# Optimization experiments

Hardware: AMD Instinct MI355X
Metric: run time of the kernel (lower is better)

The kernel has to match this reference:

```python
import jax, jax.numpy as jnp
import numpy as np

B, C, H, W = 4, 64, 128, 128

def conv1x1(x, w, b):
    # x: [B,Ci,H,W], w: [Co,Ci], b: [Co]
    return jnp.einsum('bchw,oc->bohw', x, w) + b[None, :, None, None]

def setup_inputs() -> dict:
    key = jax.random.key(0)
    ks = jax.random.split(key, 10)
    d = {}
    d['x'] = jax.random.normal(ks[0], (B, C, H, W), dtype=jnp.float32)
    # patchmerging params: LayerNorm(4C) + Linear(4C -> C)
    d['pm_gamma'] = jnp.ones((4 * C,), jnp.float32)
    d['pm_beta'] = jnp.zeros((4 * C,), jnp.float32)
    d['pm_w'] = jax.random.normal(ks[1], (C, 4 * C), jnp.float32) * 0.02
    d['pm_b'] = jnp.zeros((C,), jnp.float32)
    # 1x1 convs: conv2..conv6 are C->C, conv1 is 2C->C
    for i, n in enumerate(['2', '3', '4', '5', '6']):
        d['w' + n] = jax.random.normal(ks[2 + i], (C, C), jnp.float32) * 0.05
        d['b' + n] = jnp.zeros((C,), jnp.float32)
    d['w1'] = jax.random.normal(ks[7], (C, 2 * C), jnp.float32) * 0.05
    d['b1'] = jnp.zeros((C,), jnp.float32)
    return d

def reference(x, pm_gamma, pm_beta, pm_w, pm_b,
              w1, b1, w2, b2, w3, b3, w4, b4, w5, b5, w6, b6):
    Bx, Cx, Hx, Wx = x.shape
    Hh, Wh = Hx // 2, Wx // 2
    N = Hh * Wh
    # ---- patch merging ----
    x0 = x[:, :, 0::2, 0::2]
    x1_ = x[:, :, 1::2, 0::2]
    x2_ = x[:, :, 0::2, 1::2]
    x3_ = x[:, :, 1::2, 1::2]
    m = jnp.concatenate([x0, x1_, x2_, x3_], axis=1)        # [B,4C,Hh,Wh]
    t = m.reshape(Bx, 4 * Cx, N).transpose(0, 2, 1)          # [B,N,4C]
    mu = t.mean(-1, keepdims=True)
    var = t.var(-1, keepdims=True)
    t = (t - mu) / jnp.sqrt(var + 1e-5) * pm_gamma + pm_beta  # LayerNorm eps=1e-5
    t = t @ pm_w.T + pm_b                                     # [B,N,C]
    c1 = t.transpose(0, 2, 1).reshape(Bx, Cx, Hh, Wh)
    # ---- spatial attention (PAM-style) ----
    q = conv1x1(c1, w2, b2).reshape(Bx, Cx, N)
    k = conv1x1(c1, w3, b3).reshape(Bx, Cx, N)
    v = conv1x1(c1, w4, b4).reshape(Bx, Cx, N)
    qk1 = jax.nn.softmax(jnp.einsum('bcn,bcm->bnm', q, k), axis=-1)  # [B,N,N]
    # torch: out1 = v @ qk1.permute(0,2,1) -> out1[b,c,j] = sum_i v[b,c,i]*qk1[b,j,i]
    out1 = jnp.einsum('bci,bji->bcj', v, qk1).reshape(Bx, Cx, Hh, Wh)
    # ---- channel attention (CAM-style) ----
    q2 = conv1x1(c1, w5, b5).reshape(Bx, Cx, N)
    k2 = conv1x1(c1, w6, b6).reshape(Bx, Cx, N)
    qk2 = jax.nn.softmax(jnp.einsum('bcn,bdn->bcd', q2, k2), axis=-1)  # [B,C,C]
    out2 = jnp.einsum('bcd,bdn->bcn', qk2, v).reshape(Bx, Cx, Hh, Wh)
    # ---- fuse, 1x1 conv, bilinear upsample x2 (align_corners=False), residual ----
    out = jnp.concatenate([out1, out2], axis=1)              # [B,2C,Hh,Wh]
    out = conv1x1(out, w1, b1)                               # [B,C,Hh,Wh]
    out = jax.image.resize(out, (Bx, Cx, Hx, Wx), method='bilinear')
    return out + x
```

## Files before the change

### kernel.cpp

```cpp
#include <hip/hip_runtime.h>

typedef __attribute__((ext_vector_type(8))) short bf16x8;
typedef __attribute__((ext_vector_type(4))) float fx4;

struct __attribute__((aligned(8))) sh4 { short x, y, z, w; };

#define OPART_B   0u
#define ML_B      8388608u
#define SMALL_B   8650752u
#define L2M_B     12845056u
#define C1B_B     12910592u
#define QB_B      15007744u
#define KB_B      17104896u
#define VCN_B     19202048u
#define VNC_B     21299200u
#define Q2B_B     23396352u
#define K2B_B     25493504u
#define CATB_B    27590656u
#define P2B_B     31784960u
#define PMB_B     31817728u
#define W2B_B     31850496u
#define W3B_B     31858688u
#define W4B_B     31866880u
#define W5B_B     31875072u
#define W6B_B     31883264u
#define W1B_B     31891456u

static __device__ __forceinline__ short f2bf(float f) {
  unsigned u = __float_as_uint(f);
  unsigned r = (u + 0x7FFFu + ((u >> 16) & 1u)) >> 16;
  return (short)r;
}
static __device__ __forceinline__ float bf2f(short s) {
  return __uint_as_float(((unsigned)(unsigned short)s) << 16);
}

__global__ __launch_bounds__(256) void prep_kernel(
    const float* __restrict__ pm_w, const float* __restrict__ w2,
    const float* __restrict__ w3,  const float* __restrict__ w4,
    const float* __restrict__ w5,  const float* __restrict__ w6,
    const float* __restrict__ w1,  char* __restrict__ wsb)
{
  int tid = blockIdx.x * 256 + threadIdx.x;
  ((short*)(wsb + PMB_B))[tid] = f2bf(pm_w[tid]);
  if (tid < 4096) {
    ((short*)(wsb + W2B_B))[tid] = f2bf(w2[tid]);
    ((short*)(wsb + W3B_B))[tid] = f2bf(w3[tid]);
    ((short*)(wsb + W4B_B))[tid] = f2bf(w4[tid]);
    ((short*)(wsb + W5B_B))[tid] = f2bf(w5[tid]);
    ((short*)(wsb + W6B_B))[tid] = f2bf(w6[tid]);
  }
  if (tid < 8192) ((short*)(wsb + W1B_B))[tid] = f2bf(w1[tid]);
  ((float*)(wsb + L2M_B))[tid] = 0.0f;
}

__global__ __launch_bounds__(256) void patchln_kernel(
    const float* __restrict__ x, const float* __restrict__ gamma,
    const float* __restrict__ beta, const short* __restrict__ pmb,
    const float* __restrict__ pm_b, short* __restrict__ c1b)
{
  __shared__ short tnb[32*264];
  __shared__ float red_s[512];
  __shared__ float mu_s[32], rs_s[32];
  const int b   = blockIdx.y;
  const int i   = blockIdx.x >> 1;
  const int jh  = blockIdx.x & 1;
  const int tid = threadIdx.x;
  const int j   = tid & 31;
  const int g8  = tid >> 5;
  const int jj  = jh*32 + j;

  float vals[32];
  float sm = 0.f, sq = 0.f;
  #pragma unroll
  for (int k = 0; k < 16; ++k) {
    int p  = g8*16 + k;
    int cc = p & 63, di = p >> 6;
    float2 v2 = *(const float2*)&x[((size_t)(b*64 + cc)*128 + 2*i + di)*128 + 2*jj];
    vals[2*k]   = v2.x;
    vals[2*k+1] = v2.y;
    sm += v2.x + v2.y; sq += v2.x*v2.x + v2.y*v2.y;
  }
  red_s[g8*32 + j] = sm;
  red_s[256 + g8*32 + j] = sq;
  __syncthreads();
  if (tid < 32) {
    float s0 = 0.f, q0 = 0.f;
    #pragma unroll
    for (int g = 0; g < 8; ++g) { s0 += red_s[g*32 + tid]; q0 += red_s[256 + g*32 + tid]; }
    float mu  = s0 * (1.0f/256.0f);
    float var = q0 * (1.0f/256.0f) - mu*mu;
    mu_s[tid] = mu;
    rs_s[tid] = rsqrtf(var + 1e-5f);
  }
  __syncthreads();
  {
    float mu = mu_s[j], rs = rs_s[j];
    #pragma unroll
    for (int k = 0; k < 16; ++k) {
      int p  = g8*16 + k;
      int ca = p, cb = p + 128;
      tnb[j*264 + ca] = f2bf((vals[2*k]   - mu)*rs*gamma[ca] + beta[ca]);
      tnb[j*264 + cb] = f2bf((vals[2*k+1] - mu)*rs*gamma[cb] + beta[cb]);
    }
  }
  __syncthreads();

  const int w    = tid >> 6;
  const int lane = tid & 63;
  const int L15  = lane & 15;
  const int quad = lane >> 4;
  fx4 d0 = {0.f,0.f,0.f,0.f}, d1 = {0.f,0.f,0.f,0.f};
  #pragma unroll
  for (int kc = 0; kc < 8; ++kc) {
    bf16x8 a  = *(const bf16x8*)&pmb[(w*16 + L15)*256 + kc*32 + quad*8];
    bf16x8 bf0 = *(const bf16x8*)&tnb[(L15)*264      + kc*32 + quad*8];
    bf16x8 bf1 = *(const bf16x8*)&tnb[(16 + L15)*264 + kc*32 + quad*8];
    d0 = __builtin_amdgcn_mfma_f32_16x16x32_bf16(a, bf0, d0, 0, 0, 0);
    d1 = __builtin_amdgcn_mfma_f32_16x16x32_bf16(a, bf1, d1, 0, 0, 0);
  }
  const int obase = w*16 + quad*4;
  float bias0 = pm_b[obase], bias1 = pm_b[obase+1], bias2 = pm_b[obase+2], bias3 = pm_b[obase+3];
  const int gn0 = i*64 + jh*32 + L15;
  sh4 s0; s0.x = f2bf(d0[0]+bias0); s0.y = f2bf(d0[1]+bias1); s0.z = f2bf(d0[2]+bias2); s0.w = f2bf(d0[3]+bias3);
  sh4 s1; s1.x = f2bf(d1[0]+bias0); s1.y = f2bf(d1[1]+bias1); s1.z = f2bf(d1[2]+bias2); s1.w = f2bf(d1[3]+bias3);
  *(sh4*)&c1b[((size_t)b*4096 + gn0)*64 + obase]      = s0;
  *(sh4*)&c1b[((size_t)b*4096 + gn0 + 16)*64 + obase] = s1;
}

__global__ __launch_bounds__(256) void proj5_kernel(
    const short* __restrict__ c1b,
    const short* __restrict__ w2b, const short* __restrict__ w3b, const short* __restrict__ w4b,
    const short* __restrict__ w5b, const short* __restrict__ w6b,
    const float* __restrict__ b2, const float* __restrict__ b3, const float* __restrict__ b4,
    const float* __restrict__ b5, const float* __restrict__ b6,
    short* __restrict__ qb, short* __restrict__ kb,
    short* __restrict__ vcn, short* __restrict__ vnc,
    short* __restrict__ q2b, short* __restrict__ k2b)
{
  const int b    = blockIdx.y;
  const int tid  = threadIdx.x;
  const int w    = tid >> 6;
  const int nsub = w & 1;
  const int pg   = w >> 1;
  const int lane = tid & 63;
  const int L15  = lane & 15;
  const int quad = lane >> 4;
  const int gn   = blockIdx.x*32 + nsub*16 + L15;

  bf16x8 bf0 = *(const bf16x8*)&c1b[((size_t)b*4096 + gn)*64 + quad*8];
  bf16x8 bf1 = *(const bf16x8*)&c1b[((size_t)b*4096 + gn)*64 + quad*8 + 32];

  if (pg == 0) {
    const short* wp[3] = {w2b, w3b, w4b};
    const float* bp[3] = {b2, b3, b4};
    #pragma unroll
    for (int p = 0; p < 3; ++p) {
      #pragma unroll
      for (int mt = 0; mt < 4; ++mt) {
        bf16x8 a0 = *(const bf16x8*)&wp[p][(mt*16 + L15)*64 + quad*8];
        bf16x8 a1 = *(const bf16x8*)&wp[p][(mt*16 + L15)*64 + quad*8 + 32];
        fx4 d = {0.f,0.f,0.f,0.f};
        d = __builtin_amdgcn_mfma_f32_16x16x32_bf16(a0, bf0, d, 0, 0, 0);
        d = __builtin_amdgcn_mfma_f32_16x16x32_bf16(a1, bf1, d, 0, 0, 0);
        const int obase = mt*16 + quad*4;
        float r0 = d[0] + bp[p][obase];
        float r1 = d[1] + bp[p][obase+1];
        float r2 = d[2] + bp[p][obase+2];
        float r3 = d[3] + bp[p][obase+3];
        sh4 s; s.x = f2bf(r0); s.y = f2bf(r1); s.z = f2bf(r2); s.w = f2bf(r3);
        short* dst = (p == 0) ? qb : (p == 1) ? kb : vnc;
        *(sh4*)&dst[((size_t)b*4096 + gn)*64 + obase] = s;
        if (p == 2) {
          vcn[((size_t)b*64 + obase + 0)*4096 + gn] = s.x;
          vcn[((size_t)b*64 + obase + 1)*4096 + gn] = s.y;
          vcn[((size_t)b*64 + obase + 2)*4096 + gn] = s.z;
          vcn[((size_t)b*64 + obase + 3)*4096 + gn] = s.w;
        }
      }
    }
  } else {
    const short* wp[2] = {w5b, w6b};
    const float* bp[2] = {b5, b6};
    #pragma unroll
    for (int p = 0; p < 2; ++p) {
      short* dst = (p == 0) ? q2b : k2b;
      #pragma unroll
      for (int mt = 0; mt < 4; ++mt) {
        bf16x8 a0 = *(const bf16x8*)&wp[p][(mt*16 + L15)*64 + quad*8];
        bf16x8 a1 = *(const bf16x8*)&wp[p][(mt*16 + L15)*64 + quad*8 + 32];
        fx4 d = {0.f,0.f,0.f,0.f};
        d = __builtin_amdgcn_mfma_f32_16x16x32_bf16(a0, bf0, d, 0, 0, 0);
        d = __builtin_amdgcn_mfma_f32_16x16x32_bf16(a1, bf1, d, 0, 0, 0);
        const int obase = mt*16 + quad*4;
        dst[((size_t)b*64 + obase + 0)*4096 + gn] = f2bf(d[0] + bp[p][obase]);
        dst[((size_t)b*64 + obase + 1)*4096 + gn] = f2bf(d[1] + bp[p][obase+1]);
        dst[((size_t)b*64 + obase + 2)*4096 + gn] = f2bf(d[2] + bp[p][obase+2]);
        dst[((size_t)b*64 + obase + 3)*4096 + gn] = f2bf(d[3] + bp[p][obase+3]);
      }
    }
  }
}

__global__ __launch_bounds__(256) void flash_mfma_kernel(
    const short* __restrict__ Qb, const short* __restrict__ Kb,
    const short* __restrict__ Vb, short* __restrict__ opart, float* __restrict__ lsum)
{
  __shared__ short lds_s[20480];
  short* ktb = lds_s;
  short* vsb = lds_s + 8192;
  short* ps  = lds_s + 16384;

  const int b    = blockIdx.z;
  const int s    = blockIdx.y;
  const int q0   = blockIdx.x << 6;
  const int t0   = s << 4;
  const int tid  = threadIdx.x;
  const int w    = tid >> 6;
  const int lane = tid & 63;
  const int L15  = lane & 15;
  const int quad = lane >> 4;

  const short* Qg = Qb + (size_t)b*4096*64;
  const short* Kg = Kb + (size_t)b*4096*64;
  const short* Vg = Vb + (size_t)b*4096*64;

  bf16x8 qa0 = *(const bf16x8*)(Qg + (size_t)(q0 + w*16 + L15)*64 + quad*8);
  bf16x8 qa1 = *(const bf16x8*)(Qg + (size_t)(q0 + w*16 + L15)*64 + quad*8 + 32);

  bf16x8 ones;
  #pragma unroll
  for (int u = 0; u < 8; ++u) ones[u] = (short)0x3F80;

  const int si  = tid >> 2;
  const int scb = (tid & 3) * 2;
  const int s0k = scb ^ (si & 7);
  const int s1k = s0k ^ 1;

  {
    const int i0 = t0 << 6;
    bf16x8 kr0 = *(const bf16x8*)(Kg + (size_t)(i0 + si)*64 + scb*8);
    bf16x8 kr1 = *(const bf16x8*)(Kg + (size_t)(i0 + si)*64 + scb*8 + 8);
    bf16x8 vr0 = *(const bf16x8*)(Vg + (size_t)si*4096 + i0 + (tid&3)*16);
    bf16x8 vr1 = *(const bf16x8*)(Vg + (size_t)si*4096 + i0 + (tid&3)*16 + 8);
    *(bf16x8*)(ktb + si*64 + s0k*8) = kr0;
    *(bf16x8*)(ktb + si*64 + s1k*8) = kr1;
    *(bf16x8*)(vsb + si*64 + s0k*8) = vr0;
    *(bf16x8*)(vsb + si*64 + s1k*8) = vr1;
  }
  __syncthreads();

  fx4 oacc[4] = {{0.f,0.f,0.f,0.f},{0.f,0.f,0.f,0.f},{0.f,0.f,0.f,0.f},{0.f,0.f,0.f,0.f}};
  fx4 lacc   = {0.f,0.f,0.f,0.f};

  const int cbx0 = quad       ^ (L15 & 7);
  const int cbx1 = (quad + 4) ^ (L15 & 7);
  const int jq   = (quad*4) & 7;

  for (int t = 0; t < 16; ++t) {
    const short* kt = ktb + (t & 1)*4096;
    const short* vv = vsb + (t & 1)*4096;
    short* ktn = ktb + ((t + 1) & 1)*4096;
    short* vsn = vsb + ((t + 1) & 1)*4096;

    bf16x8 kr0, kr1, vr0, vr1;
    const bool pf = (t < 15);
    if (pf) {
      const int i0n = (t0 + t + 1) << 6;
      kr0 = *(const bf16x8*)(Kg + (size_t)(i0n + si)*64 + scb*8);
      kr1 = *(const bf16x8*)(Kg + (size_t)(i0n + si)*64 + scb*8 + 8);
      vr0 = *(const bf16x8*)(Vg + (size_t)si*4096 + i0n + (tid&3)*16);
      vr1 = *(const bf16x8*)(Vg + (size_t)si*4096 + i0n + (tid&3)*16 + 8);
    }

    fx4 sreg[4] = {{0.f,0.f,0.f,0.f},{0.f,0.f,0.f,0.f},{0.f,0.f,0.f,0.f},{0.f,0.f,0.f,0.f}};
    #pragma unroll
    for (int nt = 0; nt < 4; ++nt) {
      bf16x8 bk = *(const bf16x8*)(kt + (nt*16 + L15)*64 + cbx0*8);
      sreg[nt] = __builtin_amdgcn_mfma_f32_16x16x32_bf16(qa0, bk, sreg[nt], 0, 0, 0);
    }
    #pragma unroll
    for (int nt = 0; nt < 4; ++nt) {
      bf16x8 bk = *(const bf16x8*)(kt + (nt*16 + L15)*64 + cbx1*8);
      sreg[nt] = __builtin_amdgcn_mfma_f32_16x16x32_bf16(qa1, bk, sreg[nt], 0, 0, 0);
    }

    #pragma unroll
    for (int r = 0; r < 4; ++r) {
      const int j   = w*16 + quad*4 + r;
      const int js  = (jq + r) & 7;
      #pragma unroll
      for (int nt = 0; nt < 4; ++nt) {
        float e = __expf(sreg[nt][r]);
        const int slot = (nt*2 + (L15 >> 3)) ^ js;
        ps[j*64 + slot*8 + (L15 & 7)] = f2bf(e);
      }
    }

    bf16x8 pa0 = *(const bf16x8*)(ps + (w*16 + L15)*64 + (( quad      ^ (L15 & 7))*8));
    bf16x8 pa1 = *(const bf16x8*)(ps + (w*16 + L15)*64 + (((quad + 4) ^ (L15 & 7))*8));

    lacc = __builtin_amdgcn_mfma_f32_16x16x32_bf16(pa0, ones, lacc, 0, 0, 0);
    lacc = __builtin_amdgcn_mfma_f32_16x16x32_bf16(pa1, ones, lacc, 0, 0, 0);

    #pragma unroll
    for (int ct = 0; ct < 4; ++ct) {
      bf16x8 vb0 = *(const bf16x8*)(vv + (ct*16 + L15)*64 + cbx0*8);
      oacc[ct] = __builtin_amdgcn_mfma_f32_16x16x32_bf16(pa0, vb0, oacc[ct], 0, 0, 0);
      bf16x8 vb1 = *(const bf16x8*)(vv + (ct*16 + L15)*64 + cbx1*8);
      oacc[ct] = __builtin_amdgcn_mfma_f32_16x16x32_bf16(pa1, vb1, oacc[ct], 0, 0, 0);
    }

    if (pf) {
      *(bf16x8*)(ktn + si*64 + s0k*8) = kr0;
      *(bf16x8*)(ktn + si*64 + s1k*8) = kr1;
      *(bf16x8*)(vsn + si*64 + s0k*8) = vr0;
      *(bf16x8*)(vsn + si*64 + s1k*8) = vr1;
    }
    __syncthreads();
  }

  const size_t rowbase = ((size_t)(b*4 + s)*4096 + q0);
  #pragma unroll
  for (int ct = 0; ct < 4; ++ct) {
    #pragma unroll
    for (int r = 0; r < 4; ++r) {
      opart[(rowbase + w*16 + quad*4 + r)*64 + ct*16 + L15] = f2bf(oacc[ct][r]);
    }
  }
  if (L15 == 0) {
    #pragma unroll
    for (int r = 0; r < 4; ++r) {
      lsum[rowbase + w*16 + quad*4 + r] = lacc[r];
    }
  }
}

__global__ __launch_bounds__(256) void merge_kernel(
    const short* __restrict__ opart, const float* __restrict__ lsum, short* __restrict__ catb)
{
  int g  = blockIdx.x*256 + threadIdx.x;
  int b  = g >> 14;
  int r  = g & 16383;
  int n  = r >> 2;
  int c0 = (r & 3) * 16;
  float l0 = lsum[((size_t)(b*4 + 0)*4096) + n];
  float l1 = lsum[((size_t)(b*4 + 1)*4096) + n];
  float l2 = lsum[((size_t)(b*4 + 2)*4096) + n];
  float l3 = lsum[((size_t)(b*4 + 3)*4096) + n];
  float invL = 1.0f / (l0 + l1 + l2 + l3);
  bf16x8 oa, ob;
  float va[8] = {0,0,0,0,0,0,0,0}, vb[8] = {0,0,0,0,0,0,0,0};
  #pragma unroll
  for (int sp = 0; sp < 4; ++sp) {
    bf16x8 pa = *(const bf16x8*)&opart[(((size_t)(b*4+sp)*4096) + n)*64 + c0];
    bf16x8 pb = *(const bf16x8*)&opart[(((size_t)(b*4+sp)*4096) + n)*64 + c0 + 8];
    #pragma unroll
    for (int u = 0; u < 8; ++u) { va[u] += bf2f(pa[u]); vb[u] += bf2f(pb[u]); }
  }
  #pragma unroll
  for (int u = 0; u < 8; ++u) { oa[u] = f2bf(va[u]*invL); ob[u] = f2bf(vb[u]*invL); }
  *(bf16x8*)&catb[((size_t)b*4096 + n)*128 + c0]     = oa;
  *(bf16x8*)&catb[((size_t)b*4096 + n)*128 + c0 + 8] = ob;
}

__global__ __launch_bounds__(256) void corr_kernel(
    const short* __restrict__ q2b, const short* __restrict__ k2b, float* __restrict__ L2M)
{
  const int b    = blockIdx.y;
  const int n0   = blockIdx.x * 128;
  const int tid  = threadIdx.x;
  const int w    = tid >> 6;
  const int lane = tid & 63;
  const int L15  = lane & 15;
  const int quad = lane >> 4;
  const short* qg = q2b + (size_t)b*64*4096;
  const short* kg = k2b + (size_t)b*64*4096;
  fx4 D[4] = {{0.f,0.f,0.f,0.f},{0.f,0.f,0.f,0.f},{0.f,0.f,0.f,0.f},{0.f,0.f,0.f,0.f}};
  #pragma unroll
  for (int kc = 0; kc < 4; ++kc) {
    bf16x8 a = *(const bf16x8*)&qg[(w*16 + L15)*4096 + n0 + kc*32 + quad*8];
    #pragma unroll
    for (int nt = 0; nt < 4; ++nt) {
      bf16x8 bb = *(const bf16x8*)&kg[(nt*16 + L15)*4096 + n0 + kc*32 + quad*8];
      D[nt] = __builtin_amdgcn_mfma_f32_16x16x32_bf16(a, bb, D[nt], 0, 0, 0);
    }
  }
  float* Lb = L2M + (size_t)b*4096;
  #pragma unroll
  for (int nt = 0; nt < 4; ++nt)
    #pragma unroll
    for (int r = 0; r < 4; ++r)
      atomicAdd(&Lb[(w*16 + quad*4 + r)*64 + nt*16 + L15], D[nt][r]);
}

__global__ __launch_bounds__(64) void softmax64_kernel(
    const float* __restrict__ L, short* __restrict__ p2b)
{
  const int b = blockIdx.y, c = blockIdx.x, d = threadIdx.x;
  float v = L[(size_t)b*4096 + c*64 + d];
  float mx = v;
  mx = fmaxf(mx, __shfl_xor(mx, 1));
  mx = fmaxf(mx, __shfl_xor(mx, 2));
  mx = fmaxf(mx, __shfl_xor(mx, 4));
  mx = fmaxf(mx, __shfl_xor(mx, 8));
  mx = fmaxf(mx, __shfl_xor(mx, 16));
  mx = fmaxf(mx, __shfl_xor(mx, 32));
  float e = __expf(v - mx);
  float sm = e;
  sm += __shfl_xor(sm, 1);
  sm += __shfl_xor(sm, 2);
  sm += __shfl_xor(sm, 4);
  sm += __shfl_xor(sm, 8);
  sm += __shfl_xor(sm, 16);
  sm += __shfl_xor(sm, 32);
  p2b[(size_t)b*4096 + c*64 + d] = f2bf(e / sm);
}

__global__ __launch_bounds__(256) void out2_kernel(
    const short* __restrict__ p2b, const short* __restrict__ vnc, short* __restrict__ catb)
{
  const int b    = blockIdx.y;
  const int tid  = threadIdx.x;
  const int w    = tid >> 6;
  const int nsub = w & 1;
  const int mh   = w >> 1;
  const int lane = tid & 63;
  const int L15  = lane & 15;
  const int quad = lane >> 4;
  const int gn   = blockIdx.x*32 + nsub*16 + L15;

  bf16x8 bf0 = *(const bf16x8*)&vnc[((size_t)b*4096 + gn)*64 + quad*8];
  bf16x8 bf1 = *(const bf16x8*)&vnc[((size_t)b*4096 + gn)*64 + quad*8 + 32];
  #pragma unroll
  for (int mi = 0; mi < 2; ++mi) {
    const int mt = mh*2 + mi;
    bf16x8 a0 = *(const bf16x8*)&p2b[(size_t)b*4096 + (mt*16 + L15)*64 + quad*8];
    bf16x8 a1 = *(const bf16x8*)&p2b[(size_t)b*4096 + (mt*16 + L15)*64 + quad*8 + 32];
    fx4 d = {0.f,0.f,0.f,0.f};
    d = __builtin_amdgcn_mfma_f32_16x16x32_bf16(a0, bf0, d, 0, 0, 0);
    d = __builtin_amdgcn_mfma_f32_16x16x32_bf16(a1, bf1, d, 0, 0, 0);
    sh4 sv; sv.x = f2bf(d[0]); sv.y = f2bf(d[1]); sv.z = f2bf(d[2]); sv.w = f2bf(d[3]);
    *(sh4*)&catb[((size_t)b*4096 + gn)*128 + 64 + mt*16 + quad*4] = sv;
  }
}

__global__ __launch_bounds__(256) void conv_kernel(
    const short* __restrict__ catb, const short* __restrict__ w1b,
    const float* __restrict__ b1, float* __restrict__ sml)
{
  const int b    = blockIdx.y;
  const int tid  = threadIdx.x;
  const int w    = tid >> 6;
  const int nsub = w & 1;
  const int mh   = w >> 1;
  const int lane = tid & 63;
  const int L15  = lane & 15;
  const int quad = lane >> 4;
  const int gn   = blockIdx.x*32 + nsub*16 + L15;

  bf16x8 bfr[4];
  #pragma unroll
  for (int kc = 0; kc < 4; ++kc)
    bfr[kc] = *(const bf16x8*)&catb[((size_t)b*4096 + gn)*128 + kc*32 + quad*8];
  #pragma unroll
  for (int mi = 0; mi < 2; ++mi) {
    const int mt = mh*2 + mi;
    fx4 d = {0.f,0.f,0.f,0.f};
    #pragma unroll
    for (int kc = 0; kc < 4; ++kc) {
      bf16x8 a = *(const bf16x8*)&w1b[(mt*16 + L15)*128 + kc*32 + quad*8];
      d = __builtin_amdgcn_mfma_f32_16x16x32_bf16(a, bfr[kc], d, 0, 0, 0);
    }
    const int obase = mt*16 + quad*4;
    #pragma unroll
    for (int r = 0; r < 4; ++r)
      sml[((size_t)b*64 + obase + r)*4096 + gn] = d[r] + b1[obase + r];
  }
}

__global__ __launch_bounds__(256) void upsample_kernel(
    const float* __restrict__ sml, const float* __restrict__ x, float* __restrict__ out)
{
  int idx = blockIdx.x*256 + threadIdx.x;
  int J  = idx & 127;
  int I  = (idx >> 7) & 127;
  int bo = idx >> 14;
  int ih = I >> 1, jh = J >> 1;
  int i0, i1, j0, j1; float wi0, wi1, wj0, wj1;
  if (I & 1) { i0 = ih;                 i1 = (ih < 63) ? ih+1 : 63; wi0 = 0.75f; wi1 = 0.25f; }
  else       { i0 = (ih > 0) ? ih-1 : 0; i1 = ih;                   wi0 = 0.25f; wi1 = 0.75f; }
  if (J & 1) { j0 = jh;                 j1 = (jh < 63) ? jh+1 : 63; wj0 = 0.75f; wj1 = 0.25f; }
  else       { j0 = (jh > 0) ? jh-1 : 0; j1 = jh;                   wj0 = 0.25f; wj1 = 0.75f; }
  const float* sp = sml + (size_t)bo*4096;
  float r0 = wj0*sp[i0*64 + j0] + wj1*sp[i0*64 + j1];
  float r1 = wj0*sp[i1*64 + j0] + wj1*sp[i1*64 + j1];
  out[idx] = wi0*r0 + wi1*r1 + x[idx];
}

extern "C" void kernel_launch(void* const* d_in, const int* in_sizes, int n_in,
                              void* d_out, int out_size, void* d_ws, size_t ws_size,
                              hipStream_t stream) {
  const float* x     = (const float*)d_in[0];
  const float* gamma = (const float*)d_in[1];
  const float* beta  = (const float*)d_in[2];
  const float* pm_w  = (const float*)d_in[3];
  const float* pm_b  = (const float*)d_in[4];
  const float* w2 = (const float*)d_in[5];  const float* b2 = (const float*)d_in[6];
  const float* w3 = (const float*)d_in[7];  const float* b3 = (const float*)d_in[8];
  const float* w4 = (const float*)d_in[9];  const float* b4 = (const float*)d_in[10];
  const float* w5 = (const float*)d_in[11]; const float* b5 = (const float*)d_in[12];
  const float* w6 = (const float*)d_in[13]; const float* b6 = (const float*)d_in[14];
  const float* w1 = (const float*)d_in[15]; const float* b1 = (const float*)d_in[16];
  char* wsb  = (char*)d_ws;
  float* out = (float*)d_out;

  short* opart = (short*)(wsb + OPART_B);
  float* lsum  = (float*)(wsb + ML_B);
  float* sml   = (float*)(wsb + SMALL_B);
  float* l2m   = (float*)(wsb + L2M_B);
  short* c1b   = (short*)(wsb + C1B_B);
  short* qb    = (short*)(wsb + QB_B);
  short* kb    = (short*)(wsb + KB_B);
  short* vcn   = (short*)(wsb + VCN_B);
  short* vnc   = (short*)(wsb + VNC_B);
  short* q2b   = (short*)(wsb + Q2B_B);
  short* k2b   = (short*)(wsb + K2B_B);
  short* catb  = (short*)(wsb + CATB_B);
  short* p2b   = (short*)(wsb + P2B_B);
  short* pmb   = (short*)(wsb + PMB_B);
  short* w2b   = (short*)(wsb + W2B_B);
  short* w3b   = (short*)(wsb + W3B_B);
  short* w4b   = (short*)(wsb + W4B_B);
  short* w5b   = (short*)(wsb + W5B_B);
  short* w6b   = (short*)(wsb + W6B_B);
  short* w1b   = (short*)(wsb + W1B_B);

  prep_kernel<<<dim3(64), dim3(256), 0, stream>>>(pm_w, w2, w3, w4, w5, w6, w1, wsb);
  patchln_kernel<<<dim3(128,4), dim3(256), 0, stream>>>(x, gamma, beta, pmb, pm_b, c1b);
  proj5_kernel<<<dim3(128,4), dim3(256), 0, stream>>>(c1b, w2b, w3b, w4b, w5b, w6b,
      b2, b3, b4, b5, b6, qb, kb, vcn, vnc, q2b, k2b);
  flash_mfma_kernel<<<dim3(64,4,4), dim3(256), 0, stream>>>(qb, kb, vcn, opart, lsum);
  merge_kernel<<<dim3(256), dim3(256), 0, stream>>>(opart, lsum, catb);
  corr_kernel<<<dim3(32,4), dim3(256), 0, stream>>>(q2b, k2b, l2m);
  softmax64_kernel<<<dim3(64,4), dim3(64), 0, stream>>>(l2m, p2b);
  out2_kernel<<<dim3(128,4), dim3(256), 0, stream>>>(p2b, vnc, catb);
  conv_kernel<<<dim3(128,4), dim3(256), 0, stream>>>(catb, w1b, b1, sml);
  upsample_kernel<<<dim3(16384), dim3(256), 0, stream>>>(sml, x, out);
}
```

Measured before the change: 174.0 us.

## Restructure flash attention tiling and fuse merge, out2 and conv into tail kernel

The flash kernel now gives each block 128 query rows, each warp 32, and splits the KV range 8 ways instead of 4. K and V are read straight from global memory, with no LDS staging, double buffering or per-tile barriers, and the P/V operand roles are swapped so opart is written with vectorized stores. The merge, out2 and conv1x1 kernels are fused into a single tail kernel that builds the concat tile in LDS and writes the small output as bf16 in NC layout. The upsample then reads that bf16 buffer with strided gathers. This cuts launches and intermediate global traffic, at the cost of more partial-sum traffic, uncached global K/V reads, an extra bf16 rounding of the conv output, and a less accurate float-to-bf16 conversion for the exp values.

```diff
diff --git a/kernel.cpp b/kernel.cpp
--- a/kernel.cpp
+++ b/kernel.cpp
@@ -6,30 +6,32 @@
 struct __attribute__((aligned(8))) sh4 { short x, y, z, w; };
 
 #define OPART_B   0u
-#define ML_B      8388608u
-#define SMALL_B   8650752u
-#define L2M_B     12845056u
-#define C1B_B     12910592u
-#define QB_B      15007744u
-#define KB_B      17104896u
-#define VCN_B     19202048u
-#define VNC_B     21299200u
-#define Q2B_B     23396352u
-#define K2B_B     25493504u
-#define CATB_B    27590656u
-#define P2B_B     31784960u
-#define PMB_B     31817728u
-#define W2B_B     31850496u
-#define W3B_B     31858688u
-#define W4B_B     31866880u
-#define W5B_B     31875072u
-#define W6B_B     31883264u
-#define W1B_B     31891456u
+#define LSUM_B    16777216u
+#define SMALL_B   17301504u
+#define L2M_B     19398656u
+#define C1B_B     19464192u
+#define QB_B      21561344u
+#define KB_B      23658496u
+#define VCN_B     25755648u
+#define VNC_B     27852800u
+#define Q2B_B     29949952u
+#define K2B_B     32047104u
+#define P2B_B     34144256u
+#define PMB_B     34177024u
+#define W2B_B     34209792u
+#define W3B_B     34217984u
+#define W4B_B     34226176u
+#define W5B_B     34234368u
+#define W6B_B     34242560u
+#define W1B_B     34250752u
 
 static __device__ __forceinline__ short f2bf(float f) {
   unsigned u = __float_as_uint(f);
   unsigned r = (u + 0x7FFFu + ((u >> 16) & 1u)) >> 16;
   return (short)r;
+}
+static __device__ __forceinline__ short f2bf_fast(float f) {
+  return (short)((__float_as_uint(f) + 0x8000u) >> 16);
 }
 static __device__ __forceinline__ float bf2f(short s) {
   return __uint_as_float(((unsigned)(unsigned short)s) << 16);
@@ -202,166 +204,116 @@
   }
 }
 
-__global__ __launch_bounds__(256) void flash_mfma_kernel(
+__global__ __launch_bounds__(256) void flash_kernel(
     const short* __restrict__ Qb, const short* __restrict__ Kb,
-    const short* __restrict__ Vb, short* __restrict__ opart, float* __restrict__ lsum)
-{
-  __shared__ short lds_s[20480];
-  short* ktb = lds_s;
-  short* vsb = lds_s + 8192;
-  short* ps  = lds_s + 16384;
-
+    const short* __restrict__ Vcn, short* __restrict__ opart, float* __restrict__ lsum)
+{
+  __shared__ short ps[8192];
   const int b    = blockIdx.z;
   const int s    = blockIdx.y;
-  const int q0   = blockIdx.x << 6;
-  const int t0   = s << 4;
+  const int q0   = blockIdx.x << 7;
   const int tid  = threadIdx.x;
   const int w    = tid >> 6;
   const int lane = tid & 63;
   const int L15  = lane & 15;
   const int quad = lane >> 4;
-
-  const short* Qg = Qb + (size_t)b*4096*64;
-  const short* Kg = Kb + (size_t)b*4096*64;
-  const short* Vg = Vb + (size_t)b*4096*64;
-
-  bf16x8 qa0 = *(const bf16x8*)(Qg + (size_t)(q0 + w*16 + L15)*64 + quad*8);
-  bf16x8 qa1 = *(const bf16x8*)(Qg + (size_t)(q0 + w*16 + L15)*64 + quad*8 + 32);
+  const int jbase = w*32;
+
+  const short* Qg = Qb  + (size_t)b*262144;
+  const short* Kg = Kb  + (size_t)b*262144;
+  const short* Vg = Vcn + (size_t)b*262144;
+
+  bf16x8 qa[2][2];
+  #pragma unroll
+  for (int jt = 0; jt < 2; ++jt)
+    #pragma unroll
+    for (int h = 0; h < 2; ++h)
+      qa[jt][h] = *(const bf16x8*)(Qg + (size_t)(q0 + jbase + jt*16 + L15)*64 + h*32 + quad*8);
 
   bf16x8 ones;
   #pragma unroll
   for (int u = 0; u < 8; ++u) ones[u] = (short)0x3F80;
 
-  const int si  = tid >> 2;
-  const int scb = (tid & 3) * 2;
-  const int s0k = scb ^ (si & 7);
-  const int s1k = s0k ^ 1;
-
-  {
-    const int i0 = t0 << 6;
-    bf16x8 kr0 = *(const bf16x8*)(Kg + (size_t)(i0 + si)*64 + scb*8);
-    bf16x8 kr1 = *(const bf16x8*)(Kg + (size_t)(i0 + si)*64 + scb*8 + 8);
-    bf16x8 vr0 = *(const bf16x8*)(Vg + (size_t)si*4096 + i0 + (tid&3)*16);
-    bf16x8 vr1 = *(const bf16x8*)(Vg + (size_t)si*4096 + i0 + (tid&3)*16 + 8);
-    *(bf16x8*)(ktb + si*64 + s0k*8) = kr0;
-    *(bf16x8*)(ktb + si*64 + s1k*8) = kr1;
-    *(bf16x8*)(vsb + si*64 + s0k*8) = vr0;
-    *(bf16x8*)(vsb + si*64 + s1k*8) = vr1;
-  }
-  __syncthreads();
-
-  fx4 oacc[4] = {{0.f,0.f,0.f,0.f},{0.f,0.f,0.f,0.f},{0.f,0.f,0.f,0.f},{0.f,0.f,0.f,0.f}};
-  fx4 lacc   = {0.f,0.f,0.f,0.f};
-
-  const int cbx0 = quad       ^ (L15 & 7);
-  const int cbx1 = (quad + 4) ^ (L15 & 7);
-  const int jq   = (quad*4) & 7;
-
-  for (int t = 0; t < 16; ++t) {
-    const short* kt = ktb + (t & 1)*4096;
-    const short* vv = vsb + (t & 1)*4096;
-    short* ktn = ktb + ((t + 1) & 1)*4096;
-    short* vsn = vsb + ((t + 1) & 1)*4096;
-
-    bf16x8 kr0, kr1, vr0, vr1;
-    const bool pf = (t < 15);
-    if (pf) {
-      const int i0n = (t0 + t + 1) << 6;
-      kr0 = *(const bf16x8*)(Kg + (size_t)(i0n + si)*64 + scb*8);
-      kr1 = *(const bf16x8*)(Kg + (size_t)(i0n + si)*64 + scb*8 + 8);
-      vr0 = *(const bf16x8*)(Vg + (size_t)si*4096 + i0n + (tid&3)*16);
-      vr1 = *(const bf16x8*)(Vg + (size_t)si*4096 + i0n + (tid&3)*16 + 8);
-    }
-
-    fx4 sreg[4] = {{0.f,0.f,0.f,0.f},{0.f,0.f,0.f,0.f},{0.f,0.f,0.f,0.f},{0.f,0.f,0.f,0.f}};
+  fx4 oacc[2][4];
+  #pragma unroll
+  for (int jt = 0; jt < 2; ++jt)
+    #pragma unroll
+    for (int ct = 0; ct < 4; ++ct) oacc[jt][ct] = (fx4){0.f,0.f,0.f,0.f};
+  fx4 lacc[2] = {{0.f,0.f,0.f,0.f},{0.f,0.f,0.f,0.f}};
+
+  for (int t = 0; t < 8; ++t) {
+    const int i0 = (s*8 + t) << 6;
+
+    fx4 sreg[2][4];
+    #pragma unroll
+    for (int jt = 0; jt < 2; ++jt)
+      #pragma unroll
+      for (int nt = 0; nt < 4; ++nt) sreg[jt][nt] = (fx4){0.f,0.f,0.f,0.f};
     #pragma unroll
     for (int nt = 0; nt < 4; ++nt) {
-      bf16x8 bk = *(const bf16x8*)(kt + (nt*16 + L15)*64 + cbx0*8);
-      sreg[nt] = __builtin_amdgcn_mfma_f32_16x16x32_bf16(qa0, bk, sreg[nt], 0, 0, 0);
-    }
-    #pragma unroll
-    for (int nt = 0; nt < 4; ++nt) {
-      bf16x8 bk = *(const bf16x8*)(kt + (nt*16 + L15)*64 + cbx1*8);
-      sreg[nt] = __builtin_amdgcn_mfma_f32_16x16x32_bf16(qa1, bk, sreg[nt], 0, 0, 0);
-    }
-
-    #pragma unroll
-    for (int r = 0; r < 4; ++r) {
-      const int j   = w*16 + quad*4 + r;
-      const int js  = (jq + r) & 7;
-      #pragma unroll
-      for (int nt = 0; nt < 4; ++nt) {
-        float e = __expf(sreg[nt][r]);
-        const int slot = (nt*2 + (L15 >> 3)) ^ js;
-        ps[j*64 + slot*8 + (L15 & 7)] = f2bf(e);
+      const short* kp = Kg + (size_t)(i0 + nt*16 + L15)*64 + quad*8;
+      bf16x8 bk0 = *(const bf16x8*)kp;
+      bf16x8 bk1 = *(const bf16x8*)(kp + 32);
+      sreg[0][nt] = __builtin_amdgcn_mfma_f32_16x16x32_bf16(qa[0][0], bk0, sreg[0][nt], 0, 0, 0);
+      sreg[1][nt] = __builtin_amdgcn_mfma_f32_16x16x32_bf16(qa[1][0], bk0, sreg[1][nt], 0, 0, 0);
+      sreg[0][nt] = __builtin_amdgcn_mfma_f32_16x16x32_bf16(qa[0][1], bk1, sreg[0][nt], 0, 0, 0);
+      sreg[1][nt] = __builtin_amdgcn_mfma_f32_16x16x32_bf16(qa[1][1], bk1, sreg[1][nt], 0, 0, 0);
+    }
+
+    #pragma unroll
+    for (int jt = 0; jt < 2; ++jt)
+      #pragma unroll
+      for (int r = 0; r < 4; ++r) {
+        const int j  = jbase + jt*16 + quad*4 + r;
+        const int jk = j & 7;
+        #pragma unroll
+        for (int nt = 0; nt < 4; ++nt) {
+          float e = __expf(sreg[jt][nt][r]);
+          ps[j*64 + (((nt*2 + (L15 >> 3)) ^ jk) << 3) + (L15 & 7)] = f2bf_fast(e);
+        }
       }
-    }
-
-    bf16x8 pa0 = *(const bf16x8*)(ps + (w*16 + L15)*64 + (( quad      ^ (L15 & 7))*8));
-    bf16x8 pa1 = *(const bf16x8*)(ps + (w*16 + L15)*64 + (((quad + 4) ^ (L15 & 7))*8));
-
-    lacc = __builtin_amdgcn_mfma_f32_16x16x32_bf16(pa0, ones, lacc, 0, 0, 0);
-    lacc = __builtin_amdgcn_mfma_f32_16x16x32_bf16(pa1, ones, lacc, 0, 0, 0);
+
+    bf16x8 pb[2][2];
+    #pragma unroll
+    for (int jt = 0; jt < 2; ++jt) {
+      const int jrow = jbase + jt*16 + L15;
+      const int jk   = L15 & 7;
+      pb[jt][0] = *(const bf16x8*)&ps[jrow*64 + (((quad    ) ^ jk) << 3)];
+      pb[jt][1] = *(const bf16x8*)&ps[jrow*64 + (((quad + 4) ^ jk) << 3)];
+    }
+
+    #pragma unroll
+    for (int jt = 0; jt < 2; ++jt) {
+      lacc[jt] = __builtin_amdgcn_mfma_f32_16x16x32_bf16(ones, pb[jt][0], lacc[jt], 0, 0, 0);
+      lacc[jt] = __builtin_amdgcn_mfma_f32_16x16x32_bf16(ones, pb[jt][1], lacc[jt], 0, 0, 0);
+    }
 
     #pragma unroll
     for (int ct = 0; ct < 4; ++ct) {
-      bf16x8 vb0 = *(const bf16x8*)(vv + (ct*16 + L15)*64 + cbx0*8);
-      oacc[ct] = __builtin_amdgcn_mfma_f32_16x16x32_bf16(pa0, vb0, oacc[ct], 0, 0, 0);
-      bf16x8 vb1 = *(const bf16x8*)(vv + (ct*16 + L15)*64 + cbx1*8);
-      oacc[ct] = __builtin_amdgcn_mfma_f32_16x16x32_bf16(pa1, vb1, oacc[ct], 0, 0, 0);
-    }
-
-    if (pf) {
-      *(bf16x8*)(ktn + si*64 + s0k*8) = kr0;
-      *(bf16x8*)(ktn + si*64 + s1k*8) = kr1;
-      *(bf16x8*)(vsn + si*64 + s0k*8) = vr0;
-      *(bf16x8*)(vsn + si*64 + s1k*8) = vr1;
-    }
-    __syncthreads();
-  }
-
-  const size_t rowbase = ((size_t)(b*4 + s)*4096 + q0);
-  #pragma unroll
-  for (int ct = 0; ct < 4; ++ct) {
-    #pragma unroll
-    for (int r = 0; r < 4; ++r) {
-      opart[(rowbase + w*16 + quad*4 + r)*64 + ct*16 + L15] = f2bf(oacc[ct][r]);
-    }
-  }
-  if (L15 == 0) {
-    #pragma unroll
-    for (int r = 0; r < 4; ++r) {
-      lsum[rowbase + w*16 + quad*4 + r] = lacc[r];
-    }
-  }
-}
-
-__global__ __launch_bounds__(256) void merge_kernel(
-    const short* __restrict__ opart, const float* __restrict__ lsum, short* __restrict__ catb)
-{
-  int g  = blockIdx.x*256 + threadIdx.x;
-  int b  = g >> 14;
-  int r  = g & 16383;
-  int n  = r >> 2;
-  int c0 = (r & 3) * 16;
-  float l0 = lsum[((size_t)(b*4 + 0)*4096) + n];
-  float l1 = lsum[((size_t)(b*4 + 1)*4096) + n];
-  float l2 = lsum[((size_t)(b*4 + 2)*4096) + n];
-  float l3 = lsum[((size_t)(b*4 + 3)*4096) + n];
-  float invL = 1.0f / (l0 + l1 + l2 + l3);
-  bf16x8 oa, ob;
-  float va[8] = {0,0,0,0,0,0,0,0}, vb[8] = {0,0,0,0,0,0,0,0};
-  #pragma unroll
-  for (int sp = 0; sp < 4; ++sp) {
-    bf16x8 pa = *(const bf16x8*)&opart[(((size_t)(b*4+sp)*4096) + n)*64 + c0];
-    bf16x8 pb = *(const bf16x8*)&opart[(((size_t)(b*4+sp)*4096) + n)*64 + c0 + 8];
-    #pragma unroll
-    for (int u = 0; u < 8; ++u) { va[u] += bf2f(pa[u]); vb[u] += bf2f(pb[u]); }
-  }
-  #pragma unroll
-  for (int u = 0; u < 8; ++u) { oa[u] = f2bf(va[u]*invL); ob[u] = f2bf(vb[u]*invL); }
-  *(bf16x8*)&catb[((size_t)b*4096 + n)*128 + c0]     = oa;
-  *(bf16x8*)&catb[((size_t)b*4096 + n)*128 + c0 + 8] = ob;
+      const short* vp = Vg + (size_t)(ct*16 + L15)*4096 + i0 + quad*8;
+      bf16x8 va0 = *(const bf16x8*)vp;
+      bf16x8 va1 = *(const bf16x8*)(vp + 32);
+      #pragma unroll
+      for (int jt = 0; jt < 2; ++jt) {
+        oacc[jt][ct] = __builtin_amdgcn_mfma_f32_16x16x32_bf16(va0, pb[jt][0], oacc[jt][ct], 0, 0, 0);
+        oacc[jt][ct] = __builtin_amdgcn_mfma_f32_16x16x32_bf16(va1, pb[jt][1], oacc[jt][ct], 0, 0, 0);
+      }
+    }
+  }
+
+  const size_t srow = ((size_t)(b*8 + s)*4096) + q0;
+  #pragma unroll
+  for (int jt = 0; jt < 2; ++jt) {
+    const size_t nrow = srow + jbase + jt*16 + L15;
+    #pragma unroll
+    for (int ct = 0; ct < 4; ++ct) {
+      sh4 sv;
+      sv.x = f2bf(oacc[jt][ct][0]); sv.y = f2bf(oacc[jt][ct][1]);
+      sv.z = f2bf(oacc[jt][ct][2]); sv.w = f2bf(oacc[jt][ct][3]);
+      *(sh4*)&opart[nrow*64 + ct*16 + quad*4] = sv;
+    }
+    if (quad == 0) lsum[nrow] = lacc[jt][0];
+  }
 }
 
 __global__ __launch_bounds__(256) void corr_kernel(
@@ -374,8 +326,8 @@
   const int lane = tid & 63;
   const int L15  = lane & 15;
   const int quad = lane >> 4;
-  const short* qg = q2b + (size_t)b*64*4096;
-  const short* kg = k2b + (size_t)b*64*4096;
+  const short* qg = q2b + (size_t)b*262144;
+  const short* kg = k2b + (size_t)b*262144;
   fx4 D[4] = {{0.f,0.f,0.f,0.f},{0.f,0.f,0.f,0.f},{0.f,0.f,0.f,0.f},{0.f,0.f,0.f,0.f}};
   #pragma unroll
   for (int kc = 0; kc < 4; ++kc) {
@@ -417,84 +369,122 @@
   p2b[(size_t)b*4096 + c*64 + d] = f2bf(e / sm);
 }
 
-__global__ __launch_bounds__(256) void out2_kernel(
-    const short* __restrict__ p2b, const short* __restrict__ vnc, short* __restrict__ catb)
-{
+__global__ __launch_bounds__(256) void tail_kernel(
+    const short* __restrict__ opart, const float* __restrict__ lsum,
+    const short* __restrict__ p2b, const short* __restrict__ vnc,
+    const short* __restrict__ w1b, const float* __restrict__ b1,
+    short* __restrict__ sml)
+{
+  __shared__ short cat[8192];
   const int b    = blockIdx.y;
+  const int n0   = blockIdx.x << 6;
   const int tid  = threadIdx.x;
   const int w    = tid >> 6;
-  const int nsub = w & 1;
-  const int mh   = w >> 1;
   const int lane = tid & 63;
   const int L15  = lane & 15;
   const int quad = lane >> 4;
-  const int gn   = blockIdx.x*32 + nsub*16 + L15;
-
-  bf16x8 bf0 = *(const bf16x8*)&vnc[((size_t)b*4096 + gn)*64 + quad*8];
-  bf16x8 bf1 = *(const bf16x8*)&vnc[((size_t)b*4096 + gn)*64 + quad*8 + 32];
-  #pragma unroll
-  for (int mi = 0; mi < 2; ++mi) {
-    const int mt = mh*2 + mi;
-    bf16x8 a0 = *(const bf16x8*)&p2b[(size_t)b*4096 + (mt*16 + L15)*64 + quad*8];
-    bf16x8 a1 = *(const bf16x8*)&p2b[(size_t)b*4096 + (mt*16 + L15)*64 + quad*8 + 32];
-    fx4 d = {0.f,0.f,0.f,0.f};
-    d = __builtin_amdgcn_mfma_f32_16x16x32_bf16(a0, bf0, d, 0, 0, 0);
-    d = __builtin_amdgcn_mfma_f32_16x16x32_bf16(a1, bf1, d, 0, 0, 0);
-    sh4 sv; sv.x = f2bf(d[0]); sv.y = f2bf(d[1]); sv.z = f2bf(d[2]); sv.w = f2bf(d[3]);
-    *(sh4*)&catb[((size_t)b*4096 + gn)*128 + 64 + mt*16 + quad*4] = sv;
-  }
-}
-
-__global__ __launch_bounds__(256) void conv_kernel(
-    const short* __restrict__ catb, const short* __restrict__ w1b,
-    const float* __restrict__ b1, float* __restrict__ sml)
-{
-  const int b    = blockIdx.y;
-  const int tid  = threadIdx.x;
-  const int w    = tid >> 6;
-  const int nsub = w & 1;
-  const int mh   = w >> 1;
-  const int lane = tid & 63;
-  const int L15  = lane & 15;
-  const int quad = lane >> 4;
-  const int gn   = blockIdx.x*32 + nsub*16 + L15;
-
-  bf16x8 bfr[4];
-  #pragma unroll
-  for (int kc = 0; kc < 4; ++kc)
-    bfr[kc] = *(const bf16x8*)&catb[((size_t)b*4096 + gn)*128 + kc*32 + quad*8];
-  #pragma unroll
-  for (int mi = 0; mi < 2; ++mi) {
-    const int mt = mh*2 + mi;
-    fx4 d = {0.f,0.f,0.f,0.f};
+
+  {
+    const int nl = tid >> 2;
+    const int c0 = (tid & 3) << 4;
+    const size_t nglob = (size_t)b*32768 + (n0 + nl);
+    float l = 0.f;
+    #pragma unroll
+    for (int sp = 0; sp < 8; ++sp) l += lsum[nglob + (size_t)sp*4096];
+    const float inv = 1.0f / l;
+    float acc[16];
+    #pragma unroll
+    for (int u = 0; u < 16; ++u) acc[u] = 0.f;
+    #pragma unroll
+    for (int sp = 0; sp < 8; ++sp) {
+      const short* pp = opart + (nglob + (size_t)sp*4096)*64 + c0;
+      bf16x8 A0 = *(const bf16x8*)pp;
+      bf16x8 A1 = *(const bf16x8*)(pp + 8);
+      #pragma unroll
+      for (int u = 0; u < 8; ++u) { acc[u] += bf2f(A0[u]); acc[8+u] += bf2f(A1[u]); }
+    }
+    const int key = nl & 7;
+    #pragma unroll
+    for (int gi = 0; gi < 2; ++gi) {
+      const int g = ((c0 >> 3) + gi) ^ key;
+      sh4 s0, s1;
+      s0.x = f2bf(acc[gi*8+0]*inv); s0.y = f2bf(acc[gi*8+1]*inv);
+      s0.z = f2bf(acc[gi*8+2]*inv); s0.w = f2bf(acc[gi*8+3]*inv);
+      s1.x = f2bf(acc[gi*8+4]*inv); s1.y = f2bf(acc[gi*8+5]*inv);
+      s1.z = f2bf(acc[gi*8+6]*inv); s1.w = f2bf(acc[gi*8+7]*inv);
+      *(sh4*)&cat[nl*128 + g*8]     = s0;
+      *(sh4*)&cat[nl*128 + g*8 + 4] = s1;
+    }
+  }
+
+  {
+    const int nl  = w*16 + L15;
+    const int n   = n0 + nl;
+    const int key = L15 & 7;
+    bf16x8 vb0 = *(const bf16x8*)&vnc[((size_t)b*4096 + n)*64 + quad*8];
+    bf16x8 vb1 = *(const bf16x8*)&vnc[((size_t)b*4096 + n)*64 + quad*8 + 32];
+    #pragma unroll
+    for (int mt = 0; mt < 4; ++mt) {
+      bf16x8 a0 = *(const bf16x8*)&p2b[(size_t)b*4096 + (mt*16 + L15)*64 + quad*8];
+      bf16x8 a1 = *(const bf16x8*)&p2b[(size_t)b*4096 + (mt*16 + L15)*64 + quad*8 + 32];
+      fx4 d = {0.f,0.f,0.f,0.f};
+      d = __builtin_amdgcn_mfma_f32_16x16x32_bf16(a0, vb0, d, 0, 0, 0);
+      d = __builtin_amdgcn_mfma_f32_16x16x32_bf16(a1, vb1, d, 0, 0, 0);
+      const int c = 64 + mt*16 + quad*4;
+      const int g = (c >> 3) ^ key;
+      sh4 sv; sv.x = f2bf(d[0]); sv.y = f2bf(d[1]); sv.z = f2bf(d[2]); sv.w = f2bf(d[3]);
+      *(sh4*)&cat[nl*128 + g*8 + (quad & 1)*4] = sv;
+    }
+  }
+  __syncthreads();
+
+  {
+    const int nl  = w*16 + L15;
+    const int key = L15 & 7;
+    bf16x8 bfr[4];
     #pragma unroll
     for (int kc = 0; kc < 4; ++kc) {
-      bf16x8 a = *(const bf16x8*)&w1b[(mt*16 + L15)*128 + kc*32 + quad*8];
-      d = __builtin_amdgcn_mfma_f32_16x16x32_bf16(a, bfr[kc], d, 0, 0, 0);
-    }
-    const int obase = mt*16 + quad*4;
-    #pragma unroll
-    for (int r = 0; r < 4; ++r)
-      sml[((size_t)b*64 + obase + r)*4096 + gn] = d[r] + b1[obase + r];
+      const int g = (kc*4 + quad) ^ key;
+      bfr[kc] = *(const bf16x8*)&cat[nl*128 + g*8];
+    }
+    #pragma unroll
+    for (int mt = 0; mt < 4; ++mt) {
+      fx4 d = {0.f,0.f,0.f,0.f};
+      #pragma unroll
+      for (int kc = 0; kc < 4; ++kc) {
+        bf16x8 a = *(const bf16x8*)&w1b[(mt*16 + L15)*128 + kc*32 + quad*8];
+        d = __builtin_amdgcn_mfma_f32_16x16x32_bf16(a, bfr[kc], d, 0, 0, 0);
+      }
+      const int ob = mt*16 + quad*4;
+      sh4 sv;
+      sv.x = f2bf(d[0] + b1[ob]);   sv.y = f2bf(d[1] + b1[ob+1]);
+      sv.z = f2bf(d[2] + b1[ob+2]); sv.w = f2bf(d[3] + b1[ob+3]);
+      *(sh4*)&sml[((size_t)b*4096 + n0 + nl)*64 + ob] = sv;
+    }
   }
 }
 
 __global__ __launch_bounds__(256) void upsample_kernel(
-    const float* __restrict__ sml, const float* __restrict__ x, float* __restrict__ out)
+    const short* __restrict__ sml, const float* __restrict__ x, float* __restrict__ out)
 {
   int idx = blockIdx.x*256 + threadIdx.x;
   int J  = idx & 127;
   int I  = (idx >> 7) & 127;
   int bo = idx >> 14;
+  int b  = bo >> 6, oc = bo & 63;
   int ih = I >> 1, jh = J >> 1;
   int i0, i1, j0, j1; float wi0, wi1, wj0, wj1;
   if (I & 1) { i0 = ih;                 i1 = (ih < 63) ? ih+1 : 63; wi0 = 0.75f; wi1 = 0.25f; }
   else       { i0 = (ih > 0) ? ih-1 : 0; i1 = ih;                   wi0 = 0.25f; wi1 = 0.75f; }
   if (J & 1) { j0 = jh;                 j1 = (jh < 63) ? jh+1 : 63; wj0 = 0.75f; wj1 = 0.25f; }
   else       { j0 = (jh > 0) ? jh-1 : 0; j1 = jh;                   wj0 = 0.25f; wj1 = 0.75f; }
-  const float* sp = sml + (size_t)bo*4096;
-  float r0 = wj0*sp[i0*64 + j0] + wj1*sp[i0*64 + j1];
-  float r1 = wj0*sp[i1*64 + j0] + wj1*sp[i1*64 + j1];
+  const short* sp = sml + ((size_t)b*4096)*64 + oc;
+  float v00 = bf2f(sp[(i0*64 + j0)*64]);
+  float v01 = bf2f(sp[(i0*64 + j1)*64]);
+  float v10 = bf2f(sp[(i1*64 + j0)*64]);
+  float v11 = bf2f(sp[(i1*64 + j1)*64]);
+  float r0 = wj0*v00 + wj1*v01;
+  float r1 = wj0*v10 + wj1*v11;
   out[idx] = wi0*r0 + wi1*r1 + x[idx];
 }
 
@@ -516,8 +506,8 @@
   float* out = (float*)d_out;
 
   short* opart = (short*)(wsb + OPART_B);
-  float* lsum  = (float*)(wsb + ML_B);
-  float* sml   = (float*)(wsb + SMALL_B);
+  float* lsum  = (float*)(wsb + LSUM_B);
+  short* sml   = (short*)(wsb + SMALL_B);
   float* l2m   = (float*)(wsb + L2M_B);
   short* c1b   = (short*)(wsb + C1B_B);
   short* qb    = (short*)(wsb + QB_B);
@@ -526,7 +516,6 @@
   short* vnc   = (short*)(wsb + VNC_B);
   short* q2b   = (short*)(wsb + Q2B_B);
   short* k2b   = (short*)(wsb + K2B_B);
-  short* catb  = (short*)(wsb + CATB_B);
   short* p2b   = (short*)(wsb + P2B_B);
   short* pmb   = (short*)(wsb + PMB_B);
   short* w2b   = (short*)(wsb + W2B_B);
@@ -540,11 +529,9 @@
   patchln_kernel<<<dim3(128,4), dim3(256), 0, stream>>>(x, gamma, beta, pmb, pm_b, c1b);
   proj5_kernel<<<dim3(128,4), dim3(256), 0, stream>>>(c1b, w2b, w3b, w4b, w5b, w6b,
       b2, b3, b4, b5, b6, qb, kb, vcn, vnc, q2b, k2b);
-  flash_mfma_kernel<<<dim3(64,4,4), dim3(256), 0, stream>>>(qb, kb, vcn, opart, lsum);
-  merge_kernel<<<dim3(256), dim3(256), 0, stream>>>(opart, lsum, catb);
+  flash_kernel<<<dim3(32,8,4), dim3(256), 0, stream>>>(qb, kb, vcn, opart, lsum);
   corr_kernel<<<dim3(32,4), dim3(256), 0, stream>>>(q2b, k2b, l2m);
   softmax64_kernel<<<dim3(64,4), dim3(64), 0, stream>>>(l2m, p2b);
-  out2_kernel<<<dim3(128,4), dim3(256), 0, stream>>>(p2b, vnc, catb);
-  conv_kernel<<<dim3(128,4), dim3(256), 0, stream>>>(catb, w1b, b1, sml);
+  tail_kernel<<<dim3(64,4), dim3(256), 0, stream>>>(opart, lsum, p2b, vnc, w1b, b1, sml);
   upsample_kernel<<<dim3(16384), dim3(256), 0, stream>>>(sml, x, out);
 }
```

Result: slower. 222.0 us (+27.6%).
